# Optimization experiments

Measured on AMD Instinct MI355X. Metric: run time of the kernel, lower is better.

The kernel has to match this reference:

```python
import jax, jax.numpy as jnp
import numpy as np

B = 2048
PARAM_SHAPES = {
    'l1c0': (1, 8, 3, 3), 'l1c1': (3, 4, 8, 2), 'l1c2': (2, 4, 8, 2), 'l1c3': (2, 4, 8, 2), 'l1c4': (2, 4, 8, 1), 'b1': (8, 4, 4, 4, 4),
    'l2c0': (1, 4, 8, 2), 'l2c1': (2, 2, 4, 2), 'l2c2': (2, 2, 4, 2), 'l2c3': (2, 2, 4, 2), 'l2c4': (2, 2, 4, 1), 'b2': (4, 2, 2, 2, 2),
    'l3c0': (1, 2, 4, 2), 'l3c1': (2, 2, 2, 2), 'l3c2': (2, 2, 2, 2), 'l3c3': (2, 2, 2, 2), 'l3c4': (2, 2, 2, 1), 'b3': (2, 2, 2, 2, 2),
    'W': (2, 32), 'bl': (2,),
}

def setup_inputs():
    key = jax.random.key(0)
    ks = jax.random.split(key, len(PARAM_SHAPES) + 1)
    inp = {'x': jax.random.normal(ks[0], (B, 3, 8, 8, 8, 8), dtype=jnp.float32)}
    for k, (name, shp) in zip(ks[1:], PARAM_SHAPES.items()):
        scale = 0.5 if name[0] == 'l' and name != 'bl' else 0.1
        inp[name] = jax.random.normal(k, shp, dtype=jnp.float32) * scale
    return inp

def tt_linear(x, cores, bias):
    # y[b, m1..md] = sum_{n1..nd} W[m1..md, n1..nd] x[b, n1..nd] + bias[m1..md]
    # W is the TT-matrix with cores G_k of shape (r_{k-1}, m_k, n_k, r_k).
    b = x.shape[0]
    z = x.reshape(b, 1, -1)  # (B, rank, flat=[n_k..n_d, m_1..m_{k-1}])
    for G in cores:
        r0, m, n, r1 = G.shape
        z = jnp.einsum('brns,rmnq->bqsm', z.reshape(b, r0, n, -1), G).reshape(b, r1, -1)
    return z.reshape((b,) + bias.shape) + bias

def reference(x, l1c0, l1c1, l1c2, l1c3, l1c4, b1, l2c0, l2c1, l2c2, l2c3, l2c4, b2, l3c0, l3c1, l3c2, l3c3, l3c4, b3, W, bl):
    h = jax.nn.relu(tt_linear(x, [l1c0, l1c1, l1c2, l1c3, l1c4], b1))
    h = jax.nn.relu(tt_linear(h, [l2c0, l2c1, l2c2, l2c3, l2c4], b2))
    h = jax.nn.relu(tt_linear(h, [l3c0, l3c1, l3c2, l3c3, l3c4], b3))
    logits = h.reshape(-1, 32) @ W.T + bl  # (B, 2)
    return jax.nn.log_softmax(logits, axis=1)
```

## Files before the change

kernel.cpp:

```cpp
#include <hip/hip_runtime.h>
#include <math.h>

#define WC3  0
#define WC2  128
#define WU1  256
#define T2S  288
#define T3S  1440
#define H1O  288
#define AO   2528
#define BO   288
#define CO   1440
#define DO   1984
#define H2O  2256
#define H3O  2320
#define LDS_FLOATS 4576

__global__ void tt_setup_w3(const float* __restrict__ v0, const float* __restrict__ v1,
                            const float* __restrict__ v2, const float* __restrict__ v3,
                            const float* __restrict__ v4, float* __restrict__ w3) {
    int i = blockIdx.x * 256 + threadIdx.x;
    if (i >= 2048) return;
    int mi = i >> 6, nj = i & 63;
    int m1 = (mi >> 4) & 1, m2 = (mi >> 3) & 1, m3 = (mi >> 2) & 1, m4 = (mi >> 1) & 1, m5 = mi & 1;
    int n1 = (nj >> 4) & 3, n2 = (nj >> 3) & 1, n3 = (nj >> 2) & 1, n4 = (nj >> 1) & 1, n5 = nj & 1;
    float s = 0.f;
#pragma unroll
    for (int q1 = 0; q1 < 2; ++q1) {
        float a1 = v0[(m1 * 4 + n1) * 2 + q1];
#pragma unroll
        for (int q2 = 0; q2 < 2; ++q2) {
            float a2 = a1 * v1[((q1 * 2 + m2) * 2 + n2) * 2 + q2];
#pragma unroll
            for (int q3 = 0; q3 < 2; ++q3) {
                float a3 = a2 * v2[((q2 * 2 + m3) * 2 + n3) * 2 + q3];
#pragma unroll
                for (int q4 = 0; q4 < 2; ++q4)
                    s = fmaf(a3 * v3[((q3 * 2 + m4) * 2 + n4) * 2 + q4],
                             v4[(q4 * 2 + m5) * 2 + n5], s);
            }
        }
    }
    w3[i] = s;
}

__global__ __launch_bounds__(64, 2)
void tt_main(const float* __restrict__ x,
             const float* __restrict__ g0, const float* __restrict__ g1,
             const float* __restrict__ g2, const float* __restrict__ g3,
             const float* __restrict__ g4, const float* __restrict__ b1g,
             const float* __restrict__ u0, const float* __restrict__ u1,
             const float* __restrict__ u2, const float* __restrict__ u3,
             const float* __restrict__ u4, const float* __restrict__ b2g,
             const float* __restrict__ b3g,
             const float* __restrict__ Wmg, const float* __restrict__ blg,
             const float* __restrict__ w3g,
             float* __restrict__ out)
{
    __shared__ float smem[LDS_FLOATS];
    const int t = threadIdx.x;
    const int b = blockIdx.x;
    const float* xb = x + (size_t)b * 12288;

    float xv[32];
    {
        const float4* xq = (const float4*)xb + t * 8;
#pragma unroll
        for (int i = 0; i < 8; ++i) {
            const float4 v = xq[i];
            xv[i*4+0] = v.x; xv[i*4+1] = v.y; xv[i*4+2] = v.z; xv[i*4+3] = v.w;
        }
    }

    smem[WC3 + t] = g3[t];  smem[WC3 + 64 + t] = g3[64 + t];
    smem[WC2 + t] = g2[t];  smem[WC2 + 64 + t] = g2[64 + t];
    if (t < 32) smem[WU1 + t] = u1[t];
    __syncthreads();

    const int h = t & 1;
    const int p = t >> 1;

    float regT4[36];
#pragma unroll
    for (int i = 0; i < 36; ++i) regT4[i] = 0.f;

#pragma unroll
    for (int n1 = 0; n1 < 3; ++n1) {
#pragma unroll
        for (int n2h = 0; n2h < 2; ++n2h) {
            const int s = n1 * 2 + n2h;
            float xn[32];
            if (s < 5) {
                const float4* xq = (const float4*)xb + (s + 1) * 512 + t * 8;
#pragma unroll
                for (int i = 0; i < 8; ++i) {
                    const float4 v = xq[i];
                    xn[i*4+0] = v.x; xn[i*4+1] = v.y; xn[i*4+2] = v.z; xn[i*4+3] = v.w;
                }
            }

            float t1[32];
#pragma unroll
            for (int m5 = 0; m5 < 4; ++m5)
#pragma unroll
            for (int q4 = 0; q4 < 2; ++q4) {
                const float* w = g4 + (q4 * 4 + m5) * 8;
#pragma unroll
                for (int n4l = 0; n4l < 4; ++n4l) {
                    float sa = xv[n4l*8+0] * w[0];
#pragma unroll
                    for (int n5 = 1; n5 < 8; ++n5) sa = fmaf(xv[n4l*8+n5], w[n5], sa);
                    t1[n4l*8 + m5*2 + q4] = sa;
                }
            }

            float acc[16];
#pragma unroll
            for (int i = 0; i < 16; ++i) acc[i] = 0.f;
#pragma unroll
            for (int pass = 0; pass < 2; ++pass) {
                const int hh = (pass == 0) ? h : (1 - h);
                if (pass == 1) {
#pragma unroll
                    for (int i = 0; i < 32; ++i) t1[i] = __shfl_xor(t1[i], 1);
                }
#pragma unroll
                for (int m4 = 0; m4 < 4; ++m4) {
                    const int cbase = WC3 + ((h * 4 + m4) * 8 + hh * 4) * 2;
                    const float4 c0 = *(const float4*)&smem[cbase];
                    const float4 c1 = *(const float4*)&smem[cbase + 4];
                    const float cs[8] = {c0.x, c0.y, c0.z, c0.w, c1.x, c1.y, c1.z, c1.w};
#pragma unroll
                    for (int m5 = 0; m5 < 4; ++m5) {
                        float sa = acc[m4*4+m5];
#pragma unroll
                        for (int n4l = 0; n4l < 4; ++n4l)
#pragma unroll
                        for (int q4 = 0; q4 < 2; ++q4)
                            sa = fmaf(t1[n4l*8 + m5*2 + q4], cs[n4l*2 + q4], sa);
                        acc[m4*4+m5] = sa;
                    }
                }
            }

            __syncthreads();
#pragma unroll
            for (int m45 = 0; m45 < 16; ++m45)
                smem[T2S + p * 36 + m45 * 2 + h] = acc[m45];
            __syncthreads();

            {
                const int n3h = t & 1;
                const int q2  = (t >> 1) & 1;
                const int m3  = (t >> 2) & 3;
                const int n2l = t >> 4;
                float o3[16];
#pragma unroll
                for (int i = 0; i < 16; ++i) o3[i] = 0.f;
#pragma unroll
                for (int n3l = 0; n3l < 4; ++n3l) {
                    const int rb = T2S + (n2l * 8 + n3h * 4 + n3l) * 36;
                    float rv[32];
#pragma unroll
                    for (int g = 0; g < 8; ++g) {
                        const float4 v = *(const float4*)&smem[rb + g * 4];
                        rv[g*4+0] = v.x; rv[g*4+1] = v.y; rv[g*4+2] = v.z; rv[g*4+3] = v.w;
                    }
                    const int wb = WC2 + ((q2 * 4 + m3) * 8 + n3h * 4 + n3l) * 2;
                    const float w0 = smem[wb], w1 = smem[wb + 1];
#pragma unroll
                    for (int m45 = 0; m45 < 16; ++m45)
                        o3[m45] = fmaf(rv[m45*2], w0, fmaf(rv[m45*2+1], w1, o3[m45]));
                }
#pragma unroll
                for (int k = 0; k < 16; ++k) o3[k] += __shfl_xor(o3[k], 1);
                const int row = n2h * 16 + n2l * 4 + m3;
#pragma unroll
                for (int k = 0; k < 8; ++k) {
                    const float v = n3h ? o3[8 + k] : o3[k];
                    smem[T3S + row * 34 + (n3h * 8 + k) * 2 + q2] = v;
                }
            }
            if (s < 5) {
#pragma unroll
                for (int i = 0; i < 32; ++i) xv[i] = xn[i];
            }
        }
        __syncthreads();

        {
            const int m3 = t >> 4, m4 = (t >> 2) & 3, m5 = t & 3;
            float2 zz[8];
#pragma unroll
            for (int n2 = 0; n2 < 8; ++n2)
                zz[n2] = *(const float2*)&smem[T3S + (n2 * 4 + m3) * 34 + (m4 * 4 + m5) * 2];
#pragma unroll
            for (int jj = 0; jj < 4; ++jj)
#pragma unroll
            for (int q1 = 0; q1 < 3; ++q1) {
                float sa = regT4[jj * 9 + n1 * 3 + q1];
#pragma unroll
                for (int n2g = 0; n2g < 4; ++n2g) {
                    const float4 w = *(const float4*)(g1 + ((q1 * 4 + jj) * 8 + n2g * 2) * 2);
                    sa = fmaf(zz[n2g*2].x,   w.x, sa);
                    sa = fmaf(zz[n2g*2].y,   w.y, sa);
                    sa = fmaf(zz[n2g*2+1].x, w.z, sa);
                    sa = fmaf(zz[n2g*2+1].y, w.w, sa);
                }
                regT4[jj * 9 + n1 * 3 + q1] = sa;
            }
        }
    }
    __syncthreads();

#pragma unroll
    for (int jj = 0; jj < 4; ++jj) {
        float bia[8];
#pragma unroll
        for (int m1 = 0; m1 < 8; ++m1) bia[m1] = b1g[m1 * 256 + jj * 64 + t];
#pragma unroll
        for (int m1 = 0; m1 < 8; ++m1) {
            float sa = bia[m1];
#pragma unroll
            for (int n1 = 0; n1 < 3; ++n1)
#pragma unroll
            for (int q1 = 0; q1 < 3; ++q1)
                sa = fmaf(regT4[jj * 9 + n1 * 3 + q1], g0[(m1 * 3 + n1) * 3 + q1], sa);
            smem[H1O + m1 * 256 + jj * 64 + t] = fmaxf(sa, 0.f);
        }
    }
    __syncthreads();

#pragma unroll
    for (int pp = 0; pp < 8; ++pp) {
        const int P = pp * 64 + t;
        const float4 hv = *(const float4*)&smem[H1O + P * 4];
        float4 av;
        av.x = hv.x*u4[0]  + hv.y*u4[1]  + hv.z*u4[2]  + hv.w*u4[3];
        av.y = hv.x*u4[8]  + hv.y*u4[9]  + hv.z*u4[10] + hv.w*u4[11];
        av.z = hv.x*u4[4]  + hv.y*u4[5]  + hv.z*u4[6]  + hv.w*u4[7];
        av.w = hv.x*u4[12] + hv.y*u4[13] + hv.z*u4[14] + hv.w*u4[15];
        *(float4*)&smem[AO + P * 4] = av;
    }
    __syncthreads();

#pragma unroll
    for (int pp = 0; pp < 2; ++pp) {
        const int p3 = pp * 64 + t;
        float4 aa[4];
#pragma unroll
        for (int n4 = 0; n4 < 4; ++n4)
            aa[n4] = *(const float4*)&smem[AO + (p3 * 4 + n4) * 4];
        float o[8];
#pragma unroll
        for (int i = 0; i < 8; ++i) o[i] = 0.f;
#pragma unroll
        for (int n4 = 0; n4 < 4; ++n4)
#pragma unroll
        for (int q4 = 0; q4 < 2; ++q4) {
            const float a0 = q4 ? aa[n4].y : aa[n4].x;
            const float a1 = q4 ? aa[n4].w : aa[n4].z;
#pragma unroll
            for (int q3 = 0; q3 < 2; ++q3)
#pragma unroll
            for (int m4 = 0; m4 < 2; ++m4) {
                const float w = u3[((q3 * 2 + m4) * 4 + n4) * 2 + q4];
                o[(m4 * 2 + 0) * 2 + q3] = fmaf(a0, w, o[(m4 * 2 + 0) * 2 + q3]);
                o[(m4 * 2 + 1) * 2 + q3] = fmaf(a1, w, o[(m4 * 2 + 1) * 2 + q3]);
            }
        }
#pragma unroll
        for (int k = 0; k < 8; ++k) smem[BO + p3 * 9 + k] = o[k];
    }
    __syncthreads();

    if (t < 32) {
        float o[16];
#pragma unroll
        for (int i = 0; i < 16; ++i) o[i] = 0.f;
#pragma unroll
        for (int n3 = 0; n3 < 4; ++n3)
#pragma unroll
        for (int q3 = 0; q3 < 2; ++q3) {
            float zb[4];
#pragma unroll
            for (int m45 = 0; m45 < 4; ++m45)
                zb[m45] = smem[BO + (t * 4 + n3) * 9 + m45 * 2 + q3];
#pragma unroll
            for (int m3 = 0; m3 < 2; ++m3)
#pragma unroll
            for (int q2 = 0; q2 < 2; ++q2) {
                const float w = u2[((q2 * 2 + m3) * 4 + n3) * 2 + q3];
#pragma unroll
                for (int m45 = 0; m45 < 4; ++m45)
                    o[(m3 * 4 + m45) * 2 + q2] = fmaf(zb[m45], w, o[(m3 * 4 + m45) * 2 + q2]);
            }
        }
#pragma unroll
        for (int k = 0; k < 16; ++k) smem[CO + t * 17 + k] = o[k];
    }
    __syncthreads();

    if (t < 32) {
        const int n1 = t >> 2, m2 = (t >> 1) & 1, m3 = t & 1;
        float o[8];
#pragma unroll
        for (int i = 0; i < 8; ++i) o[i] = 0.f;
#pragma unroll
        for (int n2 = 0; n2 < 4; ++n2)
#pragma unroll
        for (int q2 = 0; q2 < 2; ++q2) {
            float cb[4];
#pragma unroll
            for (int m45 = 0; m45 < 4; ++m45)
                cb[m45] = smem[CO + (n1 * 4 + n2) * 17 + (m3 * 4 + m45) * 2 + q2];
#pragma unroll
            for (int q1 = 0; q1 < 2; ++q1) {
                const float w = smem[WU1 + ((q1 * 2 + m2) * 4 + n2) * 2 + q2];
#pragma unroll
                for (int m45 = 0; m45 < 4; ++m45)
                    o[m45 * 2 + q1] = fmaf(cb[m45], w, o[m45 * 2 + q1]);
            }
        }
#pragma unroll
        for (int m45 = 0; m45 < 4; ++m45)
#pragma unroll
        for (int q1 = 0; q1 < 2; ++q1)
            smem[DO + (m2 * 8 + m3 * 4 + m45) * 17 + n1 * 2 + q1] = o[m45 * 2 + q1];
    }
    __syncthreads();

    if (t < 16) {
        float o[4];
#pragma unroll
        for (int i = 0; i < 4; ++i) o[i] = 0.f;
#pragma unroll
        for (int n1 = 0; n1 < 8; ++n1)
#pragma unroll
        for (int q1 = 0; q1 < 2; ++q1) {
            const float dv = smem[DO + t * 17 + n1 * 2 + q1];
#pragma unroll
            for (int m1 = 0; m1 < 4; ++m1)
                o[m1] = fmaf(dv, u0[(m1 * 8 + n1) * 2 + q1], o[m1]);
        }
#pragma unroll
        for (int m1 = 0; m1 < 4; ++m1)
            smem[H2O + m1 * 16 + t] = fmaxf(o[m1] + b2g[m1 * 16 + t], 0.f);
    }
    __syncthreads();

    if (t < 32) {
        const float4* wr = (const float4*)(w3g + t * 64);
        float sa = b3g[t];
#pragma unroll
        for (int g = 0; g < 16; ++g) {
            const float4 w4 = wr[g];
            sa = fmaf(w4.x, smem[H2O + g*4 + 0],
                 fmaf(w4.y, smem[H2O + g*4 + 1],
                 fmaf(w4.z, smem[H2O + g*4 + 2],
                 fmaf(w4.w, smem[H2O + g*4 + 3], sa))));
        }
        smem[H3O + t] = fmaxf(sa, 0.f);
    }
    __syncthreads();

    {
        const int k = t & 31;
        float pr = smem[H3O + k] * Wmg[t];
#pragma unroll
        for (int d = 16; d >= 1; d >>= 1) pr += __shfl_xor(pr, d);
        const float l0 = __shfl(pr, 0) + blg[0];
        const float l1 = __shfl(pr, 32) + blg[1];
        if (t == 0) {
            const float mm = fmaxf(l0, l1);
            const float lse = mm + logf(expf(l0 - mm) + expf(l1 - mm));
            out[(size_t)b * 2 + 0] = l0 - lse;
            out[(size_t)b * 2 + 1] = l1 - lse;
        }
    }
}

extern "C" void kernel_launch(void* const* d_in, const int* in_sizes, int n_in,
                              void* d_out, int out_size, void* d_ws, size_t ws_size,
                              hipStream_t stream) {
    const float* x    = (const float*)d_in[0];
    const float* l1c0 = (const float*)d_in[1];
    const float* l1c1 = (const float*)d_in[2];
    const float* l1c2 = (const float*)d_in[3];
    const float* l1c3 = (const float*)d_in[4];
    const float* l1c4 = (const float*)d_in[5];
    const float* b1   = (const float*)d_in[6];
    const float* l2c0 = (const float*)d_in[7];
    const float* l2c1 = (const float*)d_in[8];
    const float* l2c2 = (const float*)d_in[9];
    const float* l2c3 = (const float*)d_in[10];
    const float* l2c4 = (const float*)d_in[11];
    const float* b2   = (const float*)d_in[12];
    const float* l3c0 = (const float*)d_in[13];
    const float* l3c1 = (const float*)d_in[14];
    const float* l3c2 = (const float*)d_in[15];
    const float* l3c3 = (const float*)d_in[16];
    const float* l3c4 = (const float*)d_in[17];
    const float* b3   = (const float*)d_in[18];
    const float* Wm   = (const float*)d_in[19];
    const float* bl   = (const float*)d_in[20];
    float* W3 = (float*)d_ws;

    tt_setup_w3<<<8, 256, 0, stream>>>(l3c0, l3c1, l3c2, l3c3, l3c4, W3);
    tt_main<<<2048, 64, 0, stream>>>(x, l1c0, l1c1, l1c2, l1c3, l1c4, b1,
                                     l2c0, l2c1, l2c2, l2c3, l2c4, b2, b3,
                                     Wm, bl, W3, (float*)d_out);
}
```

Measured before the change: 208.4 us.

## Split per-sample TT layer-1 work across two wavefronts per block

Launches 128 threads per sample instead of 64. Each wavefront handles one n2 half of the first TT layer using its own scratch region, with wave-local lgkmcnt waits replacing two block barriers. The first-layer accumulator registers are halved and later stages are spread over more threads. The LDS layout is reshuffled so the intermediate reuses the H1 buffer in place. The cost is more threads per sample and extra block-wide barriers in the tail stages, where many threads sit idle.

```diff
diff --git a/kernel.cpp b/kernel.cpp
--- a/kernel.cpp
+++ b/kernel.cpp
@@ -1,19 +1,19 @@
 #include <hip/hip_runtime.h>
 #include <math.h>
 
-#define WC3  0
-#define WC2  128
-#define WU1  256
-#define T2S  288
-#define T3S  1440
-#define H1O  288
-#define AO   2528
-#define BO   288
-#define CO   1440
-#define DO   1984
-#define H2O  2256
-#define H3O  2320
-#define LDS_FLOATS 4576
+#define WC3   0
+#define WC2   128
+#define WU1   256
+#define T2S0  288
+#define T2S1  1440
+#define T3S   2592
+#define H1O   288
+#define BO    2336
+#define CO    3488
+#define DO    4032
+#define H2O   4304
+#define H3O   4368
+#define LDS_FLOATS 4400
 
 __global__ void tt_setup_w3(const float* __restrict__ v0, const float* __restrict__ v1,
                             const float* __restrict__ v2, const float* __restrict__ v3,
@@ -43,7 +43,7 @@
     w3[i] = s;
 }
 
-__global__ __launch_bounds__(64, 2)
+__global__ __launch_bounds__(128, 4)
 void tt_main(const float* __restrict__ x,
              const float* __restrict__ g0, const float* __restrict__ g1,
              const float* __restrict__ g2, const float* __restrict__ g3,
@@ -57,13 +57,15 @@
              float* __restrict__ out)
 {
     __shared__ float smem[LDS_FLOATS];
-    const int t = threadIdx.x;
+    const int t   = threadIdx.x;
+    const int tl  = t & 63;
+    const int wid = t >> 6;
     const int b = blockIdx.x;
     const float* xb = x + (size_t)b * 12288;
 
     float xv[32];
     {
-        const float4* xq = (const float4*)xb + t * 8;
+        const float4* xq = (const float4*)xb + wid * 512 + tl * 8;
 #pragma unroll
         for (int i = 0; i < 8; ++i) {
             const float4 v = xq[i];
@@ -71,152 +73,152 @@
         }
     }
 
-    smem[WC3 + t] = g3[t];  smem[WC3 + 64 + t] = g3[64 + t];
-    smem[WC2 + t] = g2[t];  smem[WC2 + 64 + t] = g2[64 + t];
+    smem[WC3 + t] = g3[t];
+    smem[WC2 + t] = g2[t];
     if (t < 32) smem[WU1 + t] = u1[t];
     __syncthreads();
 
-    const int h = t & 1;
-    const int p = t >> 1;
-
-    float regT4[36];
-#pragma unroll
-    for (int i = 0; i < 36; ++i) regT4[i] = 0.f;
+    const int h = tl & 1;
+    const int p = tl >> 1;
+    const int T2W = wid ? T2S1 : T2S0;
+
+    float regT4[18];
+#pragma unroll
+    for (int i = 0; i < 18; ++i) regT4[i] = 0.f;
 
 #pragma unroll
     for (int n1 = 0; n1 < 3; ++n1) {
-#pragma unroll
-        for (int n2h = 0; n2h < 2; ++n2h) {
-            const int s = n1 * 2 + n2h;
-            float xn[32];
-            if (s < 5) {
-                const float4* xq = (const float4*)xb + (s + 1) * 512 + t * 8;
-#pragma unroll
-                for (int i = 0; i < 8; ++i) {
-                    const float4 v = xq[i];
-                    xn[i*4+0] = v.x; xn[i*4+1] = v.y; xn[i*4+2] = v.z; xn[i*4+3] = v.w;
+        float xn[32];
+        if (n1 < 2) {
+            const float4* xq = (const float4*)xb + ((n1 + 1) * 2 + wid) * 512 + tl * 8;
+#pragma unroll
+            for (int i = 0; i < 8; ++i) {
+                const float4 v = xq[i];
+                xn[i*4+0] = v.x; xn[i*4+1] = v.y; xn[i*4+2] = v.z; xn[i*4+3] = v.w;
+            }
+        }
+
+        float t1[32];
+#pragma unroll
+        for (int m5 = 0; m5 < 4; ++m5)
+#pragma unroll
+        for (int q4 = 0; q4 < 2; ++q4) {
+            const float* w = g4 + (q4 * 4 + m5) * 8;
+#pragma unroll
+            for (int n4l = 0; n4l < 4; ++n4l) {
+                float sa = xv[n4l*8+0] * w[0];
+#pragma unroll
+                for (int n5 = 1; n5 < 8; ++n5) sa = fmaf(xv[n4l*8+n5], w[n5], sa);
+                t1[n4l*8 + m5*2 + q4] = sa;
+            }
+        }
+
+        float acc[16];
+#pragma unroll
+        for (int i = 0; i < 16; ++i) acc[i] = 0.f;
+#pragma unroll
+        for (int pass = 0; pass < 2; ++pass) {
+            const int hh = (pass == 0) ? h : (1 - h);
+            if (pass == 1) {
+#pragma unroll
+                for (int i = 0; i < 32; ++i) t1[i] = __shfl_xor(t1[i], 1);
+            }
+#pragma unroll
+            for (int m4 = 0; m4 < 4; ++m4) {
+                const int cbase = WC3 + ((h * 4 + m4) * 8 + hh * 4) * 2;
+                const float4 c0 = *(const float4*)&smem[cbase];
+                const float4 c1 = *(const float4*)&smem[cbase + 4];
+                const float cs[8] = {c0.x, c0.y, c0.z, c0.w, c1.x, c1.y, c1.z, c1.w};
+#pragma unroll
+                for (int m5 = 0; m5 < 4; ++m5) {
+                    float sa = acc[m4*4+m5];
+#pragma unroll
+                    for (int n4l = 0; n4l < 4; ++n4l)
+#pragma unroll
+                    for (int q4 = 0; q4 < 2; ++q4)
+                        sa = fmaf(t1[n4l*8 + m5*2 + q4], cs[n4l*2 + q4], sa);
+                    acc[m4*4+m5] = sa;
                 }
             }
-
-            float t1[32];
-#pragma unroll
-            for (int m5 = 0; m5 < 4; ++m5)
-#pragma unroll
-            for (int q4 = 0; q4 < 2; ++q4) {
-                const float* w = g4 + (q4 * 4 + m5) * 8;
-#pragma unroll
-                for (int n4l = 0; n4l < 4; ++n4l) {
-                    float sa = xv[n4l*8+0] * w[0];
-#pragma unroll
-                    for (int n5 = 1; n5 < 8; ++n5) sa = fmaf(xv[n4l*8+n5], w[n5], sa);
-                    t1[n4l*8 + m5*2 + q4] = sa;
+        }
+
+        asm volatile("s_waitcnt lgkmcnt(0)" ::: "memory");
+#pragma unroll
+        for (int m45 = 0; m45 < 16; ++m45)
+            smem[T2W + p * 36 + m45 * 2 + h] = acc[m45];
+        asm volatile("s_waitcnt lgkmcnt(0)" ::: "memory");
+
+        {
+            const int n3h = tl & 1;
+            const int q2  = (tl >> 1) & 1;
+            const int m3  = (tl >> 2) & 3;
+            const int n2l = tl >> 4;
+            float o3[16];
+#pragma unroll
+            for (int i = 0; i < 16; ++i) o3[i] = 0.f;
+#pragma unroll
+            for (int n3l = 0; n3l < 4; ++n3l) {
+                const int rb = T2W + (n2l * 8 + n3h * 4 + n3l) * 36;
+                float rv[32];
+#pragma unroll
+                for (int g = 0; g < 8; ++g) {
+                    const float4 v = *(const float4*)&smem[rb + g * 4];
+                    rv[g*4+0] = v.x; rv[g*4+1] = v.y; rv[g*4+2] = v.z; rv[g*4+3] = v.w;
                 }
-            }
-
-            float acc[16];
-#pragma unroll
-            for (int i = 0; i < 16; ++i) acc[i] = 0.f;
-#pragma unroll
-            for (int pass = 0; pass < 2; ++pass) {
-                const int hh = (pass == 0) ? h : (1 - h);
-                if (pass == 1) {
-#pragma unroll
-                    for (int i = 0; i < 32; ++i) t1[i] = __shfl_xor(t1[i], 1);
-                }
-#pragma unroll
-                for (int m4 = 0; m4 < 4; ++m4) {
-                    const int cbase = WC3 + ((h * 4 + m4) * 8 + hh * 4) * 2;
-                    const float4 c0 = *(const float4*)&smem[cbase];
-                    const float4 c1 = *(const float4*)&smem[cbase + 4];
-                    const float cs[8] = {c0.x, c0.y, c0.z, c0.w, c1.x, c1.y, c1.z, c1.w};
-#pragma unroll
-                    for (int m5 = 0; m5 < 4; ++m5) {
-                        float sa = acc[m4*4+m5];
-#pragma unroll
-                        for (int n4l = 0; n4l < 4; ++n4l)
-#pragma unroll
-                        for (int q4 = 0; q4 < 2; ++q4)
-                            sa = fmaf(t1[n4l*8 + m5*2 + q4], cs[n4l*2 + q4], sa);
-                        acc[m4*4+m5] = sa;
-                    }
-                }
-            }
-
-            __syncthreads();
-#pragma unroll
-            for (int m45 = 0; m45 < 16; ++m45)
-                smem[T2S + p * 36 + m45 * 2 + h] = acc[m45];
-            __syncthreads();
-
-            {
-                const int n3h = t & 1;
-                const int q2  = (t >> 1) & 1;
-                const int m3  = (t >> 2) & 3;
-                const int n2l = t >> 4;
-                float o3[16];
-#pragma unroll
-                for (int i = 0; i < 16; ++i) o3[i] = 0.f;
-#pragma unroll
-                for (int n3l = 0; n3l < 4; ++n3l) {
-                    const int rb = T2S + (n2l * 8 + n3h * 4 + n3l) * 36;
-                    float rv[32];
-#pragma unroll
-                    for (int g = 0; g < 8; ++g) {
-                        const float4 v = *(const float4*)&smem[rb + g * 4];
-                        rv[g*4+0] = v.x; rv[g*4+1] = v.y; rv[g*4+2] = v.z; rv[g*4+3] = v.w;
-                    }
-                    const int wb = WC2 + ((q2 * 4 + m3) * 8 + n3h * 4 + n3l) * 2;
-                    const float w0 = smem[wb], w1 = smem[wb + 1];
-#pragma unroll
-                    for (int m45 = 0; m45 < 16; ++m45)
-                        o3[m45] = fmaf(rv[m45*2], w0, fmaf(rv[m45*2+1], w1, o3[m45]));
-                }
-#pragma unroll
-                for (int k = 0; k < 16; ++k) o3[k] += __shfl_xor(o3[k], 1);
-                const int row = n2h * 16 + n2l * 4 + m3;
-#pragma unroll
-                for (int k = 0; k < 8; ++k) {
-                    const float v = n3h ? o3[8 + k] : o3[k];
-                    smem[T3S + row * 34 + (n3h * 8 + k) * 2 + q2] = v;
-                }
-            }
-            if (s < 5) {
-#pragma unroll
-                for (int i = 0; i < 32; ++i) xv[i] = xn[i];
-            }
+                const int wb = WC2 + ((q2 * 4 + m3) * 8 + n3h * 4 + n3l) * 2;
+                const float w0 = smem[wb], w1 = smem[wb + 1];
+#pragma unroll
+                for (int m45 = 0; m45 < 16; ++m45)
+                    o3[m45] = fmaf(rv[m45*2], w0, fmaf(rv[m45*2+1], w1, o3[m45]));
+            }
+#pragma unroll
+            for (int k = 0; k < 16; ++k) o3[k] += __shfl_xor(o3[k], 1);
+            const int row = wid * 16 + n2l * 4 + m3;
+#pragma unroll
+            for (int k = 0; k < 8; ++k) {
+                const float v = n3h ? o3[8 + k] : o3[k];
+                smem[T3S + row * 34 + (n3h * 8 + k) * 2 + q2] = v;
+            }
+        }
+        if (n1 < 2) {
+#pragma unroll
+            for (int i = 0; i < 32; ++i) xv[i] = xn[i];
         }
         __syncthreads();
 
         {
-            const int m3 = t >> 4, m4 = (t >> 2) & 3, m5 = t & 3;
+            const int m3 = tl >> 4, m4 = (tl >> 2) & 3, m5 = tl & 3;
             float2 zz[8];
 #pragma unroll
             for (int n2 = 0; n2 < 8; ++n2)
                 zz[n2] = *(const float2*)&smem[T3S + (n2 * 4 + m3) * 34 + (m4 * 4 + m5) * 2];
 #pragma unroll
-            for (int jj = 0; jj < 4; ++jj)
-#pragma unroll
-            for (int q1 = 0; q1 < 3; ++q1) {
-                float sa = regT4[jj * 9 + n1 * 3 + q1];
-#pragma unroll
-                for (int n2g = 0; n2g < 4; ++n2g) {
-                    const float4 w = *(const float4*)(g1 + ((q1 * 4 + jj) * 8 + n2g * 2) * 2);
-                    sa = fmaf(zz[n2g*2].x,   w.x, sa);
-                    sa = fmaf(zz[n2g*2].y,   w.y, sa);
-                    sa = fmaf(zz[n2g*2+1].x, w.z, sa);
-                    sa = fmaf(zz[n2g*2+1].y, w.w, sa);
+            for (int j = 0; j < 2; ++j) {
+                const int jj = wid * 2 + j;
+#pragma unroll
+                for (int q1 = 0; q1 < 3; ++q1) {
+                    float sa = regT4[j * 9 + n1 * 3 + q1];
+#pragma unroll
+                    for (int n2g = 0; n2g < 4; ++n2g) {
+                        const float4 w = *(const float4*)(g1 + ((q1 * 4 + jj) * 8 + n2g * 2) * 2);
+                        sa = fmaf(zz[n2g*2].x,   w.x, sa);
+                        sa = fmaf(zz[n2g*2].y,   w.y, sa);
+                        sa = fmaf(zz[n2g*2+1].x, w.z, sa);
+                        sa = fmaf(zz[n2g*2+1].y, w.w, sa);
+                    }
+                    regT4[j * 9 + n1 * 3 + q1] = sa;
                 }
-                regT4[jj * 9 + n1 * 3 + q1] = sa;
-            }
-        }
-    }
-    __syncthreads();
-
-#pragma unroll
-    for (int jj = 0; jj < 4; ++jj) {
+            }
+        }
+        __syncthreads();
+    }
+
+#pragma unroll
+    for (int j = 0; j < 2; ++j) {
+        const int jj = wid * 2 + j;
         float bia[8];
 #pragma unroll
-        for (int m1 = 0; m1 < 8; ++m1) bia[m1] = b1g[m1 * 256 + jj * 64 + t];
+        for (int m1 = 0; m1 < 8; ++m1) bia[m1] = b1g[m1 * 256 + jj * 64 + tl];
 #pragma unroll
         for (int m1 = 0; m1 < 8; ++m1) {
             float sa = bia[m1];
@@ -224,32 +226,31 @@
             for (int n1 = 0; n1 < 3; ++n1)
 #pragma unroll
             for (int q1 = 0; q1 < 3; ++q1)
-                sa = fmaf(regT4[jj * 9 + n1 * 3 + q1], g0[(m1 * 3 + n1) * 3 + q1], sa);
-            smem[H1O + m1 * 256 + jj * 64 + t] = fmaxf(sa, 0.f);
-        }
-    }
-    __syncthreads();
-
-#pragma unroll
-    for (int pp = 0; pp < 8; ++pp) {
-        const int P = pp * 64 + t;
-        const float4 hv = *(const float4*)&smem[H1O + P * 4];
+                sa = fmaf(regT4[j * 9 + n1 * 3 + q1], g0[(m1 * 3 + n1) * 3 + q1], sa);
+            smem[H1O + m1 * 256 + jj * 64 + tl] = fmaxf(sa, 0.f);
+        }
+    }
+    __syncthreads();
+
+#pragma unroll
+    for (int pp = 0; pp < 4; ++pp) {
+        const int P = pp * 128 + t;
+        float4* ap = (float4*)&smem[H1O + P * 4];
+        const float4 hv = *ap;
         float4 av;
         av.x = hv.x*u4[0]  + hv.y*u4[1]  + hv.z*u4[2]  + hv.w*u4[3];
         av.y = hv.x*u4[8]  + hv.y*u4[9]  + hv.z*u4[10] + hv.w*u4[11];
         av.z = hv.x*u4[4]  + hv.y*u4[5]  + hv.z*u4[6]  + hv.w*u4[7];
         av.w = hv.x*u4[12] + hv.y*u4[13] + hv.z*u4[14] + hv.w*u4[15];
-        *(float4*)&smem[AO + P * 4] = av;
-    }
-    __syncthreads();
-
-#pragma unroll
-    for (int pp = 0; pp < 2; ++pp) {
-        const int p3 = pp * 64 + t;
+        *ap = av;
+    }
+    __syncthreads();
+
+    {
         float4 aa[4];
 #pragma unroll
         for (int n4 = 0; n4 < 4; ++n4)
-            aa[n4] = *(const float4*)&smem[AO + (p3 * 4 + n4) * 4];
+            aa[n4] = *(const float4*)&smem[H1O + (t * 4 + n4) * 4];
         float o[8];
 #pragma unroll
         for (int i = 0; i < 8; ++i) o[i] = 0.f;
@@ -269,7 +270,7 @@
             }
         }
 #pragma unroll
-        for (int k = 0; k < 8; ++k) smem[BO + p3 * 9 + k] = o[k];
+        for (int k = 0; k < 8; ++k) smem[BO + t * 9 + k] = o[k];
     }
     __syncthreads();
 
@@ -363,7 +364,7 @@
     }
     __syncthreads();
 
-    {
+    if (t < 64) {
         const int k = t & 31;
         float pr = smem[H3O + k] * Wmg[t];
 #pragma unroll
@@ -406,7 +407,7 @@
     float* W3 = (float*)d_ws;
 
     tt_setup_w3<<<8, 256, 0, stream>>>(l3c0, l3c1, l3c2, l3c3, l3c4, W3);
-    tt_main<<<2048, 64, 0, stream>>>(x, l1c0, l1c1, l1c2, l1c3, l1c4, b1,
-                                     l2c0, l2c1, l2c2, l2c3, l2c4, b2, b3,
-                                     Wm, bl, W3, (float*)d_out);
+    tt_main<<<2048, 128, 0, stream>>>(x, l1c0, l1c1, l1c2, l1c3, l1c4, b1,
+                                      l2c0, l2c1, l2c2, l2c3, l2c4, b2, b3,
+                                      Wm, bl, W3, (float*)d_out);
 }
```

Result: slower. 214.2 us (+2.8%).

## Double-buffer LDS stages to drop barriers and fuse layer-2 first two cores

Applied to the files above, without the earlier changes.

Double-buffers the T2 and T3 shared-memory scratch regions (ping-pong by step parity) so two of the per-step __syncthreads calls inside the layer-1 loop can be removed. The next x slice is now loaded straight into xv after t1 is computed, which drops the separate xn register copy. Layer 2's first core (u4) is fused into the second-core loop so the AO intermediate and one barrier go away. The loop is 64 threads, i.e. one wavefront, so the barrier removal rests on lockstep execution within the wave, and LDS usage grows somewhat.

```diff
diff --git a/kernel.cpp b/kernel.cpp
--- a/kernel.cpp
+++ b/kernel.cpp
@@ -4,16 +4,17 @@
 #define WC3  0
 #define WC2  128
 #define WU1  256
-#define T2S  288
-#define T3S  1440
+#define T2A  288
+#define T2B  1440
+#define T3A  2592
+#define T3B  3680
 #define H1O  288
-#define AO   2528
-#define BO   288
-#define CO   1440
-#define DO   1984
-#define H2O  2256
-#define H3O  2320
-#define LDS_FLOATS 4576
+#define BO   2336
+#define CO   288
+#define DO   832
+#define H2O  1104
+#define H3O  1168
+#define LDS_FLOATS 4768
 
 __global__ void tt_setup_w3(const float* __restrict__ v0, const float* __restrict__ v1,
                             const float* __restrict__ v2, const float* __restrict__ v3,
@@ -85,31 +86,33 @@
 
 #pragma unroll
     for (int n1 = 0; n1 < 3; ++n1) {
+        const int T3S = (n1 & 1) ? T3B : T3A;
 #pragma unroll
         for (int n2h = 0; n2h < 2; ++n2h) {
             const int s = n1 * 2 + n2h;
-            float xn[32];
+            const int T2S = (s & 1) ? T2B : T2A;
+
+            float t1[32];
+#pragma unroll
+            for (int m5 = 0; m5 < 4; ++m5)
+#pragma unroll
+            for (int q4 = 0; q4 < 2; ++q4) {
+                const float* w = g4 + (q4 * 4 + m5) * 8;
+#pragma unroll
+                for (int n4l = 0; n4l < 4; ++n4l) {
+                    float sa = xv[n4l*8+0] * w[0];
+#pragma unroll
+                    for (int n5 = 1; n5 < 8; ++n5) sa = fmaf(xv[n4l*8+n5], w[n5], sa);
+                    t1[n4l*8 + m5*2 + q4] = sa;
+                }
+            }
+
             if (s < 5) {
                 const float4* xq = (const float4*)xb + (s + 1) * 512 + t * 8;
 #pragma unroll
                 for (int i = 0; i < 8; ++i) {
                     const float4 v = xq[i];
-                    xn[i*4+0] = v.x; xn[i*4+1] = v.y; xn[i*4+2] = v.z; xn[i*4+3] = v.w;
-                }
-            }
-
-            float t1[32];
-#pragma unroll
-            for (int m5 = 0; m5 < 4; ++m5)
-#pragma unroll
-            for (int q4 = 0; q4 < 2; ++q4) {
-                const float* w = g4 + (q4 * 4 + m5) * 8;
-#pragma unroll
-                for (int n4l = 0; n4l < 4; ++n4l) {
-                    float sa = xv[n4l*8+0] * w[0];
-#pragma unroll
-                    for (int n5 = 1; n5 < 8; ++n5) sa = fmaf(xv[n4l*8+n5], w[n5], sa);
-                    t1[n4l*8 + m5*2 + q4] = sa;
+                    xv[i*4+0] = v.x; xv[i*4+1] = v.y; xv[i*4+2] = v.z; xv[i*4+3] = v.w;
                 }
             }
 
@@ -142,11 +145,9 @@
                 }
             }
 
-            __syncthreads();
 #pragma unroll
             for (int m45 = 0; m45 < 16; ++m45)
                 smem[T2S + p * 36 + m45 * 2 + h] = acc[m45];
-            __syncthreads();
 
             {
                 const int n3h = t & 1;
@@ -180,12 +181,7 @@
                     smem[T3S + row * 34 + (n3h * 8 + k) * 2 + q2] = v;
                 }
             }
-            if (s < 5) {
-#pragma unroll
-                for (int i = 0; i < 32; ++i) xv[i] = xn[i];
-            }
-        }
-        __syncthreads();
+        }
 
         {
             const int m3 = t >> 4, m4 = (t >> 2) & 3, m5 = t & 3;
@@ -210,6 +206,7 @@
             }
         }
     }
+
     __syncthreads();
 
 #pragma unroll
@@ -231,41 +228,30 @@
     __syncthreads();
 
 #pragma unroll
-    for (int pp = 0; pp < 8; ++pp) {
-        const int P = pp * 64 + t;
-        const float4 hv = *(const float4*)&smem[H1O + P * 4];
-        float4 av;
-        av.x = hv.x*u4[0]  + hv.y*u4[1]  + hv.z*u4[2]  + hv.w*u4[3];
-        av.y = hv.x*u4[8]  + hv.y*u4[9]  + hv.z*u4[10] + hv.w*u4[11];
-        av.z = hv.x*u4[4]  + hv.y*u4[5]  + hv.z*u4[6]  + hv.w*u4[7];
-        av.w = hv.x*u4[12] + hv.y*u4[13] + hv.z*u4[14] + hv.w*u4[15];
-        *(float4*)&smem[AO + P * 4] = av;
-    }
-    __syncthreads();
-
-#pragma unroll
-    for (int pp = 0; pp < 2; ++pp) {
-        const int p3 = pp * 64 + t;
-        float4 aa[4];
-#pragma unroll
-        for (int n4 = 0; n4 < 4; ++n4)
-            aa[n4] = *(const float4*)&smem[AO + (p3 * 4 + n4) * 4];
+    for (int pq = 0; pq < 2; ++pq) {
+        const int p3 = 2 * t + pq;
         float o[8];
 #pragma unroll
         for (int i = 0; i < 8; ++i) o[i] = 0.f;
 #pragma unroll
-        for (int n4 = 0; n4 < 4; ++n4)
-#pragma unroll
-        for (int q4 = 0; q4 < 2; ++q4) {
-            const float a0 = q4 ? aa[n4].y : aa[n4].x;
-            const float a1 = q4 ? aa[n4].w : aa[n4].z;
-#pragma unroll
-            for (int q3 = 0; q3 < 2; ++q3)
-#pragma unroll
-            for (int m4 = 0; m4 < 2; ++m4) {
-                const float w = u3[((q3 * 2 + m4) * 4 + n4) * 2 + q4];
-                o[(m4 * 2 + 0) * 2 + q3] = fmaf(a0, w, o[(m4 * 2 + 0) * 2 + q3]);
-                o[(m4 * 2 + 1) * 2 + q3] = fmaf(a1, w, o[(m4 * 2 + 1) * 2 + q3]);
+        for (int n4 = 0; n4 < 4; ++n4) {
+            const float4 hv = *(const float4*)&smem[H1O + (p3 * 4 + n4) * 4];
+            const float ax = hv.x*u4[0]  + hv.y*u4[1]  + hv.z*u4[2]  + hv.w*u4[3];
+            const float ay = hv.x*u4[8]  + hv.y*u4[9]  + hv.z*u4[10] + hv.w*u4[11];
+            const float az = hv.x*u4[4]  + hv.y*u4[5]  + hv.z*u4[6]  + hv.w*u4[7];
+            const float aw = hv.x*u4[12] + hv.y*u4[13] + hv.z*u4[14] + hv.w*u4[15];
+#pragma unroll
+            for (int q4 = 0; q4 < 2; ++q4) {
+                const float a0 = q4 ? ay : ax;
+                const float a1 = q4 ? aw : az;
+#pragma unroll
+                for (int q3 = 0; q3 < 2; ++q3)
+#pragma unroll
+                for (int m4 = 0; m4 < 2; ++m4) {
+                    const float w = u3[((q3 * 2 + m4) * 4 + n4) * 2 + q4];
+                    o[(m4 * 2 + 0) * 2 + q3] = fmaf(a0, w, o[(m4 * 2 + 0) * 2 + q3]);
+                    o[(m4 * 2 + 1) * 2 + q3] = fmaf(a1, w, o[(m4 * 2 + 1) * 2 + q3]);
+                }
             }
         }
 #pragma unroll
```

Measured after the change: 222.8 us. 6.9% more time.
